# Performance work log

Hardware: AMD Instinct MI355X
Metric: run time of the kernel (lower is better)

The kernel has to match this reference:

```python
import jax, jax.numpy as jnp
import numpy as np

B, N, D = 4, 1024, 1024
H, HD = 16, 64  # num_heads, head_dim


def rotate_half(x):
    x1, x2 = jnp.split(x, 2, axis=-1)
    return jnp.concatenate([-x2, x1], axis=-1)


def setup_inputs() -> dict:
    key = jax.random.key(0)
    ks = jax.random.split(key, 10)
    s = 1.0 / np.sqrt(D)
    hidden_states = jax.random.normal(ks[0], (B, N, D), jnp.float32)
    # rotary angles -> cos/sin per position per head-dim
    ang = jax.random.uniform(ks[1], (B, N, HD), jnp.float32, 0.0, 2 * np.pi)
    cos, sin = jnp.cos(ang), jnp.sin(ang)
    wq = jax.random.normal(ks[2], (D, D), jnp.float32) * s
    bq = jnp.zeros((D,), jnp.float32)
    wk = jax.random.normal(ks[3], (D, D), jnp.float32) * s  # key_bias=False
    wv = jax.random.normal(ks[4], (D, D), jnp.float32) * s
    bv = jnp.zeros((D,), jnp.float32)
    wo = jax.random.normal(ks[5], (D, D), jnp.float32) * s
    bo = jnp.zeros((D,), jnp.float32)
    return {"hidden_states": hidden_states, "cos": cos, "sin": sin,
            "wq": wq, "bq": bq, "wk": wk, "wv": wv, "bv": bv,
            "wo": wo, "bo": bo}


def reference(hidden_states, cos, sin, wq, bq, wk, wv, bv, wo, bo):
    # weights are (out, in) as in eqx Linear: y = x @ W.T + b
    q = jnp.einsum('bnd,ed->bne', hidden_states, wq) + bq
    k = jnp.einsum('bnd,ed->bne', hidden_states, wk)
    v = jnp.einsum('bnd,ed->bne', hidden_states, wv) + bv
    # [B, H, N, HD]
    q = q.reshape(B, N, H, HD).transpose(0, 2, 1, 3)
    k = k.reshape(B, N, H, HD).transpose(0, 2, 1, 3)
    v = v.reshape(B, N, H, HD).transpose(0, 2, 1, 3)
    c = cos[:, None, :, :]  # broadcast over heads
    s = sin[:, None, :, :]
    q = q * c + rotate_half(q) * s
    k = k * c + rotate_half(k) * s
    scale = 1.0 / np.sqrt(HD)
    scores = jnp.einsum('bhqd,bhkd->bhqk', q, k) * scale
    attn = jax.nn.softmax(scores, axis=-1)
    out = jnp.einsum('bhqk,bhkd->bhqd', attn, v)
    out = out.transpose(0, 2, 1, 3).reshape(B, N, D)
    return jnp.einsum('bnd,ed->bne', out, wo) + bo
```

## Files before the change

### kernel.cpp

```cpp
#include <hip/hip_runtime.h>
#include <hip/hip_bf16.h>
#include <cstdint>


typedef _Float16 half8 __attribute__((ext_vector_type(8)));
typedef _Float16 half4 __attribute__((ext_vector_type(4)));
typedef float f32x4 __attribute__((ext_vector_type(4)));

#define DEV_INLINE __device__ __forceinline__

constexpr int Bb = 4, Ns = 1024, Dd = 1024, Hh = 16, HDd = 64;
constexpr int M_ROWS = Bb * Ns;
constexpr int EQKV = 3 * Dd;

constexpr size_t OFF_HSH  = 0;
constexpr size_t SZ_HSH   = (size_t)M_ROWS * Dd * 2;
constexpr size_t OFF_WQKV = OFF_HSH + SZ_HSH;
constexpr size_t SZ_WQKV  = (size_t)EQKV * Dd * 2;
constexpr size_t OFF_WO   = OFF_WQKV + SZ_WQKV;
constexpr size_t SZ_WO    = (size_t)Dd * Dd * 2;
constexpr size_t OFF_BIAS = OFF_WO + SZ_WO;
constexpr size_t OFF_VR   = OFF_BIAS + 16384;
constexpr size_t SZ_HEADS = (size_t)Bb * Hh * Ns * HDd * 2;
constexpr size_t OFF_QT   = OFF_VR + SZ_HEADS;
constexpr size_t OFF_KT   = OFF_QT + SZ_HEADS;
constexpr size_t OFF_VT   = OFF_KT + SZ_HEADS;
constexpr size_t OFF_ATTN = OFF_VR;

DEV_INLINE void async_cp16(const _Float16* g, _Float16* l) {
  __builtin_amdgcn_global_load_lds(
      (const __attribute__((address_space(1))) unsigned int*)(g),
      (__attribute__((address_space(3))) unsigned int*)(l), 16, 0, 0);
}

DEV_INLINE half4 cvt4(float4 v) {
  half4 h;
  h[0] = (_Float16)v.x; h[1] = (_Float16)v.y;
  h[2] = (_Float16)v.z; h[3] = (_Float16)v.w;
  return h;
}

__global__ __launch_bounds__(256) void cvt_kernel(
    const float* __restrict__ hs, const float* __restrict__ wq,
    const float* __restrict__ wk, const float* __restrict__ wv,
    const float* __restrict__ wo, const float* __restrict__ bq,
    const float* __restrict__ bv, _Float16* __restrict__ hsH,
    _Float16* __restrict__ wqkvH, _Float16* __restrict__ woH,
    float* __restrict__ biasP)
{
  const int gid = blockIdx.x * 256 + threadIdx.x;
  const int nHs4 = M_ROWS * Dd / 4;
  const int nW4  = 3 * Dd * Dd / 4;
  const int nWo4 = Dd * Dd / 4;
  if (gid < EQKV / 4) {
#pragma unroll
    for (int j = 0; j < 4; ++j) {
      int e = gid * 4 + j;
      biasP[e] = (e < 1024) ? bq[e] : (e < 2048 ? 0.f : bv[e - 2048]);
    }
  }
  if (gid < nHs4) {
    float4 v = reinterpret_cast<const float4*>(hs)[gid];
    reinterpret_cast<half4*>(hsH)[gid] = cvt4(v);
  } else if (gid < nHs4 + nW4) {
    int j = gid - nHs4;
    const int per = Dd * Dd / 4;
    const float* src = (j < per) ? wq : (j < 2 * per ? wk : wv);
    float4 v = reinterpret_cast<const float4*>(src)[j % per];
    reinterpret_cast<half4*>(wqkvH)[j] = cvt4(v);
  } else if (gid < nHs4 + nW4 + nWo4) {
    int j = gid - nHs4 - nW4;
    float4 v = reinterpret_cast<const float4*>(wo)[j];
    reinterpret_cast<half4*>(woH)[j] = cvt4(v);
  }
}

template<int MODE>
__global__ __launch_bounds__(256, 3) void gemm_bt(
    const _Float16* __restrict__ A, const _Float16* __restrict__ Bt,
    const float* __restrict__ bias, void* __restrict__ out,
    const float* __restrict__ cosp, const float* __restrict__ sinp,
    _Float16* __restrict__ qT, _Float16* __restrict__ kT,
    int M, int E, int K)
{
  __shared__ _Float16 As[128 * 64];
  __shared__ _Float16 Bs[128 * 64];
  const int t = threadIdx.x;
  const int lane = t & 63, wave = t >> 6;
  const int c15 = lane & 15, g = lane >> 4;
  const int wm = wave >> 1, wn = wave & 1;
  const int m0 = blockIdx.y * 128, e0 = blockIdx.x * 128;

  const int srow  = t >> 3;
  const int scol8 = ((t & 7) ^ ((t >> 3) & 7)) * 8;
  const _Float16* gA0 = A  + (size_t)(m0 + srow) * K + scol8;
  const _Float16* gB0 = Bt + (size_t)(e0 + srow) * K + scol8;
  char* lA = (char*)As + wave * 1024;
  char* lB = (char*)Bs + wave * 1024;

  const char* pA[4][2];
  const char* pB[4][2];
#pragma unroll
  for (int mi = 0; mi < 4; ++mi)
#pragma unroll
    for (int kh = 0; kh < 2; ++kh) {
      int ra = wm * 64 + mi * 16 + c15;
      pA[mi][kh] = (const char*)As + ra * 128 + (((kh * 4 + g) ^ (ra & 7)) << 4);
      int rb = wn * 64 + mi * 16 + c15;
      pB[mi][kh] = (const char*)Bs + rb * 128 + (((kh * 4 + g) ^ (rb & 7)) << 4);
    }

  f32x4 acc[4][4];
  const f32x4 zero = {0.f, 0.f, 0.f, 0.f};
#pragma unroll
  for (int i = 0; i < 4; ++i)
#pragma unroll
    for (int j = 0; j < 4; ++j) acc[i][j] = zero;

  const int nk = K >> 6;
  for (int kt = 0; kt < nk; ++kt) {
    const _Float16* ga = gA0 + kt * 64;
    const _Float16* gb = gB0 + kt * 64;
#pragma unroll
    for (int i = 0; i < 4; ++i) {
      async_cp16(ga + (size_t)(32 * i) * K, (_Float16*)(lA + i * 4096));
      async_cp16(gb + (size_t)(32 * i) * K, (_Float16*)(lB + i * 4096));
    }
    __syncthreads();
#pragma unroll
    for (int kh = 0; kh < 2; ++kh) {
      half8 a[4], b[4];
#pragma unroll
      for (int i = 0; i < 4; ++i) a[i] = *reinterpret_cast<const half8*>(pA[i][kh]);
#pragma unroll
      for (int i = 0; i < 4; ++i) b[i] = *reinterpret_cast<const half8*>(pB[i][kh]);
#pragma unroll
      for (int i = 0; i < 4; ++i)
#pragma unroll
        for (int j = 0; j < 4; ++j)
          acc[i][j] = __builtin_amdgcn_mfma_f32_16x16x32_f16(a[i], b[j], acc[i][j], 0, 0, 0);
    }
    __syncthreads();
  }

  if (MODE == 1) {
#pragma unroll
    for (int i = 0; i < 4; ++i)
#pragma unroll
      for (int j = 0; j < 4; ++j)
#pragma unroll
        for (int r = 0; r < 4; ++r) {
          int row = m0 + wm * 64 + i * 16 + g * 4 + r;
          int col = e0 + wn * 64 + j * 16 + c15;
          reinterpret_cast<float*>(out)[(size_t)row * E + col] =
              acc[i][j][r] + bias[col];
        }
  } else {
    const int scol = e0 + wn * 64;
    const int sec = scol >> 10;
    const int h = (scol & 1023) >> 6;
    if (sec < 2) {
      _Float16* dst = sec ? kT : qT;
#pragma unroll
      for (int i = 0; i < 4; ++i)
#pragma unroll
        for (int r = 0; r < 4; ++r) {
          int row = m0 + wm * 64 + i * 16 + g * 4 + r;
          int bh = (row >> 10) * Hh + h;
          size_t obase = ((size_t)bh * Ns + (row & 1023)) * HDd;
          const float* cb = cosp + (size_t)row * HDd;
          const float* sb = sinp + (size_t)row * HDd;
#pragma unroll
          for (int j = 0; j < 2; ++j) {
            int hd = j * 16 + c15;
            float x1 = acc[i][j][r]     + bias[scol + hd];
            float x2 = acc[i][j + 2][r] + bias[scol + hd + 32];
            float c1 = cb[hd],      s1 = sb[hd];
            float c2 = cb[hd + 32], s2 = sb[hd + 32];
            dst[obase + hd]      = (_Float16)(x1 * c1 - x2 * s1);
            dst[obase + hd + 32] = (_Float16)(x2 * c2 + x1 * s2);
          }
        }
    } else {
      _Float16* vR = (_Float16*)out;
#pragma unroll
      for (int i = 0; i < 4; ++i)
#pragma unroll
        for (int r = 0; r < 4; ++r) {
          int row = m0 + wm * 64 + i * 16 + g * 4 + r;
          int bh = (row >> 10) * Hh + h;
          size_t obase = ((size_t)bh * Ns + (row & 1023)) * HDd;
#pragma unroll
          for (int j = 0; j < 4; ++j) {
            int hd = j * 16 + c15;
            vR[obase + hd] = (_Float16)(acc[i][j][r] + bias[scol + hd]);
          }
        }
    }
  }
}

__global__ __launch_bounds__(256) void vtrans_kernel(
    const _Float16* __restrict__ vR, _Float16* __restrict__ vTo)
{
  __shared__ _Float16 Vs[64 * 72];
  const int t = threadIdx.x;
  const int bx = blockIdx.x;
  const int nt = bx & 15, bh = bx >> 4;
  const int n0 = nt * 64;
#pragma unroll
  for (int ii = 0; ii < 2; ++ii) {
    int cid = t + 256 * ii;
    int r = cid >> 3, ch = cid & 7;
    half8 v = *reinterpret_cast<const half8*>(
        vR + ((size_t)bh * Ns + n0 + r) * HDd + ch * 8);
    *reinterpret_cast<half8*>(&Vs[r * 72 + ch * 8]) = v;
  }
  __syncthreads();
#pragma unroll
  for (int ii = 0; ii < 2; ++ii) {
    int cid = t + 256 * ii;
    int d = cid >> 3, ch = cid & 7;
    half8 w;
#pragma unroll
    for (int kk = 0; kk < 8; ++kk) w[kk] = Vs[(ch * 8 + kk) * 72 + d];
    *reinterpret_cast<half8*>(vTo + ((size_t)bh * HDd + d) * Ns + n0 + ch * 8) = w;
  }
}

__global__ __launch_bounds__(256, 2) void attn_kernel(
    const _Float16* __restrict__ qT, const _Float16* __restrict__ kT,
    const _Float16* __restrict__ vT, _Float16* __restrict__ attnH)
{
  __shared__ _Float16 Ks[2][64 * 64];
  __shared__ _Float16 Vst[2][64 * 64];
  __shared__ _Float16 Ps[128 * 64];
  const int t = threadIdx.x;
  const int lane = t & 63, wave = t >> 6;
  const int c = lane & 15, g = lane >> 4;
  const int bx = blockIdx.x;
  const int qt = bx & 7, bh = bx >> 3;
  const int b = bh >> 4, h = bh & 15;
  const int qn0 = qt * 128;
  const int wq0 = wave * 32;

  half8 qf[2][2];
#pragma unroll
  for (int s16 = 0; s16 < 2; ++s16) {
    const _Float16* qp =
        qT + ((size_t)bh * Ns + qn0 + wq0 + s16 * 16 + c) * HDd + g * 8;
    qf[s16][0] = *reinterpret_cast<const half8*>(qp);
    qf[s16][1] = *reinterpret_cast<const half8*>(qp + 32);
  }

  half8 ones;
#pragma unroll
  for (int j = 0; j < 8; ++j) ones[j] = (_Float16)1.0f;

  f32x4 accO[2][4];
  f32x4 accL[2];
  const f32x4 zero = {0.f, 0.f, 0.f, 0.f};
#pragma unroll
  for (int s16 = 0; s16 < 2; ++s16) {
    accL[s16] = zero;
#pragma unroll
    for (int d = 0; d < 4; ++d) accO[s16][d] = zero;
  }

  const int srow = t >> 3, sch = t & 7;
  const int ssw = (sch * 16) ^ ((srow & 7) << 4);
  const _Float16* gK = kT + ((size_t)bh * Ns + srow) * HDd + sch * 8;
  const _Float16* gV = vT + ((size_t)bh * HDd + srow) * Ns + sch * 8;
  char* wKa = (char*)Ks[0]  + srow * 128 + ssw;
  char* wVa = (char*)Vst[0] + srow * 128 + ssw;

  const char* pK[2][4];
  const char* pV[2][4];
  const char* pP[2][2];
#pragma unroll
  for (int ks = 0; ks < 2; ++ks) {
#pragma unroll
    for (int i = 0; i < 4; ++i) {
      int rowk = i * 16 + c;
      pK[ks][i] = (const char*)Ks[0]  + rowk * 128 + ((ks * 64 + g * 16) ^ ((rowk & 7) << 4));
      pV[ks][i] = (const char*)Vst[0] + rowk * 128 + ((ks * 64 + g * 16) ^ ((rowk & 7) << 4));
    }
#pragma unroll
    for (int s16 = 0; s16 < 2; ++s16) {
      int rowp = wq0 + s16 * 16 + c;
      pP[s16][ks] = (const char*)Ps + rowp * 128 + ((ks * 64 + g * 16) ^ ((rowp & 7) << 4));
    }
  }

  const float K1 = 0.18033688011112042f;
  const float K2 = -11.541560327111707f;
  char* prow0 = (char*)Ps + (wq0 + c) * 128;
  const int psw = (c & 7) << 4;

  {
    half8 k0 = *reinterpret_cast<const half8*>(gK);
    half8 k1 = *reinterpret_cast<const half8*>(gK + 32 * HDd);
    half8 v0 = *reinterpret_cast<const half8*>(gV);
    half8 v1 = *reinterpret_cast<const half8*>(gV + 32 * Ns);
    *reinterpret_cast<half8*>(wKa) = k0;
    *reinterpret_cast<half8*>(wKa + 4096) = k1;
    *reinterpret_cast<half8*>(wVa) = v0;
    *reinterpret_cast<half8*>(wVa + 4096) = v1;
  }
  __syncthreads();

  for (int jt = 0; jt < 16; ++jt) {
    const int bo = (jt & 1) * 8192;
    const bool pre = (jt + 1 < 16);
    half8 kr0, kr1, vr0, vr1;
    if (pre) {
      kr0 = *reinterpret_cast<const half8*>(gK + (jt + 1) * 4096);
      kr1 = *reinterpret_cast<const half8*>(gK + (jt + 1) * 4096 + 32 * HDd);
      vr0 = *reinterpret_cast<const half8*>(gV + (jt + 1) * 64);
      vr1 = *reinterpret_cast<const half8*>(gV + (jt + 1) * 64 + 32 * Ns);
    }

    f32x4 s[2][4];
#pragma unroll
    for (int s16 = 0; s16 < 2; ++s16)
#pragma unroll
      for (int i = 0; i < 4; ++i) s[s16][i] = zero;
    __builtin_amdgcn_s_setprio(1);
#pragma unroll
    for (int ks = 0; ks < 2; ++ks) {
      half8 kf[4];
#pragma unroll
      for (int i = 0; i < 4; ++i)
        kf[i] = *reinterpret_cast<const half8*>(pK[ks][i] + bo);
#pragma unroll
      for (int i = 0; i < 4; ++i) {
        s[0][i] = __builtin_amdgcn_mfma_f32_16x16x32_f16(kf[i], qf[0][ks], s[0][i], 0, 0, 0);
        s[1][i] = __builtin_amdgcn_mfma_f32_16x16x32_f16(kf[i], qf[1][ks], s[1][i], 0, 0, 0);
      }
    }
    __builtin_amdgcn_s_setprio(0);

#pragma unroll
    for (int s16 = 0; s16 < 2; ++s16) {
      char* prow = prow0 + s16 * 2048;
#pragma unroll
      for (int i = 0; i < 4; ++i) {
        half4 pk;
        pk[0] = (_Float16)__builtin_amdgcn_exp2f(fmaf(s[s16][i][0], K1, K2));
        pk[1] = (_Float16)__builtin_amdgcn_exp2f(fmaf(s[s16][i][1], K1, K2));
        pk[2] = (_Float16)__builtin_amdgcn_exp2f(fmaf(s[s16][i][2], K1, K2));
        pk[3] = (_Float16)__builtin_amdgcn_exp2f(fmaf(s[s16][i][3], K1, K2));
        *reinterpret_cast<half4*>(prow + ((i * 32 + g * 8) ^ psw)) = pk;
      }
    }

    __builtin_amdgcn_s_setprio(1);
#pragma unroll
    for (int ks = 0; ks < 2; ++ks) {
      half8 pa0 = *reinterpret_cast<const half8*>(pP[0][ks]);
      half8 pa1 = *reinterpret_cast<const half8*>(pP[1][ks]);
      accL[0] = __builtin_amdgcn_mfma_f32_16x16x32_f16(pa0, ones, accL[0], 0, 0, 0);
      accL[1] = __builtin_amdgcn_mfma_f32_16x16x32_f16(pa1, ones, accL[1], 0, 0, 0);
#pragma unroll
      for (int dt = 0; dt < 4; ++dt) {
        half8 vf = *reinterpret_cast<const half8*>(pV[ks][dt] + bo);
        accO[0][dt] = __builtin_amdgcn_mfma_f32_16x16x32_f16(pa0, vf, accO[0][dt], 0, 0, 0);
        accO[1][dt] = __builtin_amdgcn_mfma_f32_16x16x32_f16(pa1, vf, accO[1][dt], 0, 0, 0);
      }
    }
    __builtin_amdgcn_s_setprio(0);

    if (pre) {
      const int wo_ = 8192 - bo;
      *reinterpret_cast<half8*>(wKa + wo_) = kr0;
      *reinterpret_cast<half8*>(wKa + wo_ + 4096) = kr1;
      *reinterpret_cast<half8*>(wVa + wo_) = vr0;
      *reinterpret_cast<half8*>(wVa + wo_ + 4096) = vr1;
      __syncthreads();
    }
  }

#pragma unroll
  for (int s16 = 0; s16 < 2; ++s16)
#pragma unroll
    for (int r = 0; r < 4; ++r) {
      float inv = 1.f / accL[s16][r];
      int n = qn0 + wq0 + s16 * 16 + g * 4 + r;
#pragma unroll
      for (int dt = 0; dt < 4; ++dt) {
        float v = accO[s16][dt][r] * inv;
        attnH[((size_t)b * Ns + n) * Dd + h * HDd + dt * 16 + c] = (_Float16)v;
      }
    }
}

extern "C" void kernel_launch(void* const* d_in, const int* in_sizes, int n_in,
                              void* d_out, int out_size, void* d_ws, size_t ws_size,
                              hipStream_t stream) {
  const float* hs   = (const float*)d_in[0];
  const float* cosp = (const float*)d_in[1];
  const float* sinp = (const float*)d_in[2];
  const float* wq   = (const float*)d_in[3];
  const float* bq   = (const float*)d_in[4];
  const float* wk   = (const float*)d_in[5];
  const float* wv   = (const float*)d_in[6];
  const float* bv   = (const float*)d_in[7];
  const float* wo   = (const float*)d_in[8];
  const float* bo   = (const float*)d_in[9];

  char* ws = (char*)d_ws;
  _Float16* hsH   = (_Float16*)(ws + OFF_HSH);
  _Float16* wqkvH = (_Float16*)(ws + OFF_WQKV);
  _Float16* woH   = (_Float16*)(ws + OFF_WO);
  float*    biasP = (float*)(ws + OFF_BIAS);
  _Float16* vRp   = (_Float16*)(ws + OFF_VR);
  _Float16* qTp   = (_Float16*)(ws + OFF_QT);
  _Float16* kTp   = (_Float16*)(ws + OFF_KT);
  _Float16* vTp   = (_Float16*)(ws + OFF_VT);
  _Float16* attnH = (_Float16*)(ws + OFF_ATTN);

  cvt_kernel<<<8192, 256, 0, stream>>>(hs, wq, wk, wv, wo, bq, bv,
                                       hsH, wqkvH, woH, biasP);
  gemm_bt<0><<<dim3(EQKV / 128, M_ROWS / 128), 256, 0, stream>>>(
      hsH, wqkvH, biasP, vRp, cosp, sinp, qTp, kTp, M_ROWS, EQKV, Dd);
  vtrans_kernel<<<Bb * Hh * (Ns / 64), 256, 0, stream>>>(vRp, vTp);
  attn_kernel<<<Bb * Hh * (Ns / 128), 256, 0, stream>>>(qTp, kTp, vTp, attnH);
  gemm_bt<1><<<dim3(Dd / 128, M_ROWS / 128), 256, 0, stream>>>(
      attnH, woH, bo, d_out, nullptr, nullptr, nullptr, nullptr,
      M_ROWS, Dd, Dd);
}
```

Before: 102.4 us.

## Fuse V transpose into QKV GEMM epilogue and narrow output GEMM tile

```diff
diff --git a/kernel.cpp b/kernel.cpp
--- a/kernel.cpp
+++ b/kernel.cpp
@@ -20,12 +20,11 @@
 constexpr size_t OFF_WO   = OFF_WQKV + SZ_WQKV;
 constexpr size_t SZ_WO    = (size_t)Dd * Dd * 2;
 constexpr size_t OFF_BIAS = OFF_WO + SZ_WO;
-constexpr size_t OFF_VR   = OFF_BIAS + 16384;
+constexpr size_t OFF_ATTN = OFF_BIAS + 16384;
 constexpr size_t SZ_HEADS = (size_t)Bb * Hh * Ns * HDd * 2;
-constexpr size_t OFF_QT   = OFF_VR + SZ_HEADS;
+constexpr size_t OFF_QT   = OFF_ATTN + SZ_HEADS;
 constexpr size_t OFF_KT   = OFF_QT + SZ_HEADS;
 constexpr size_t OFF_VT   = OFF_KT + SZ_HEADS;
-constexpr size_t OFF_ATTN = OFF_VR;
 
 DEV_INLINE void async_cp16(const _Float16* g, _Float16* l) {
   __builtin_amdgcn_global_load_lds(
@@ -75,7 +74,7 @@
   }
 }
 
-template<int MODE>
+template<int MODE, int BN>
 __global__ __launch_bounds__(256, 3) void gemm_bt(
     const _Float16* __restrict__ A, const _Float16* __restrict__ Bt,
     const float* __restrict__ bias, void* __restrict__ out,
@@ -83,13 +82,14 @@
     _Float16* __restrict__ qT, _Float16* __restrict__ kT,
     int M, int E, int K)
 {
+  constexpr int JW = BN / 32;
   __shared__ _Float16 As[128 * 64];
-  __shared__ _Float16 Bs[128 * 64];
+  __shared__ _Float16 Bs[BN * 64];
   const int t = threadIdx.x;
   const int lane = t & 63, wave = t >> 6;
   const int c15 = lane & 15, g = lane >> 4;
   const int wm = wave >> 1, wn = wave & 1;
-  const int m0 = blockIdx.y * 128, e0 = blockIdx.x * 128;
+  const int m0 = blockIdx.y * 128, e0 = blockIdx.x * BN;
 
   const int srow  = t >> 3;
   const int scol8 = ((t & 7) ^ ((t >> 3) & 7)) * 8;
@@ -99,45 +99,51 @@
   char* lB = (char*)Bs + wave * 1024;
 
   const char* pA[4][2];
-  const char* pB[4][2];
+  const char* pB[JW][2];
 #pragma unroll
   for (int mi = 0; mi < 4; ++mi)
 #pragma unroll
     for (int kh = 0; kh < 2; ++kh) {
       int ra = wm * 64 + mi * 16 + c15;
       pA[mi][kh] = (const char*)As + ra * 128 + (((kh * 4 + g) ^ (ra & 7)) << 4);
-      int rb = wn * 64 + mi * 16 + c15;
-      pB[mi][kh] = (const char*)Bs + rb * 128 + (((kh * 4 + g) ^ (rb & 7)) << 4);
-    }
-
-  f32x4 acc[4][4];
+    }
+#pragma unroll
+  for (int j = 0; j < JW; ++j)
+#pragma unroll
+    for (int kh = 0; kh < 2; ++kh) {
+      int rb = wn * (BN / 2) + j * 16 + c15;
+      pB[j][kh] = (const char*)Bs + rb * 128 + (((kh * 4 + g) ^ (rb & 7)) << 4);
+    }
+
+  f32x4 acc[4][JW];
   const f32x4 zero = {0.f, 0.f, 0.f, 0.f};
 #pragma unroll
   for (int i = 0; i < 4; ++i)
 #pragma unroll
-    for (int j = 0; j < 4; ++j) acc[i][j] = zero;
+    for (int j = 0; j < JW; ++j) acc[i][j] = zero;
 
   const int nk = K >> 6;
   for (int kt = 0; kt < nk; ++kt) {
     const _Float16* ga = gA0 + kt * 64;
     const _Float16* gb = gB0 + kt * 64;
 #pragma unroll
-    for (int i = 0; i < 4; ++i) {
+    for (int i = 0; i < 4; ++i)
       async_cp16(ga + (size_t)(32 * i) * K, (_Float16*)(lA + i * 4096));
+#pragma unroll
+    for (int i = 0; i < BN / 32; ++i)
       async_cp16(gb + (size_t)(32 * i) * K, (_Float16*)(lB + i * 4096));
-    }
     __syncthreads();
 #pragma unroll
     for (int kh = 0; kh < 2; ++kh) {
-      half8 a[4], b[4];
+      half8 a[4], b[JW];
 #pragma unroll
       for (int i = 0; i < 4; ++i) a[i] = *reinterpret_cast<const half8*>(pA[i][kh]);
 #pragma unroll
-      for (int i = 0; i < 4; ++i) b[i] = *reinterpret_cast<const half8*>(pB[i][kh]);
+      for (int j = 0; j < JW; ++j) b[j] = *reinterpret_cast<const half8*>(pB[j][kh]);
 #pragma unroll
       for (int i = 0; i < 4; ++i)
 #pragma unroll
-        for (int j = 0; j < 4; ++j)
+        for (int j = 0; j < JW; ++j)
           acc[i][j] = __builtin_amdgcn_mfma_f32_16x16x32_f16(a[i], b[j], acc[i][j], 0, 0, 0);
     }
     __syncthreads();
@@ -147,11 +153,11 @@
 #pragma unroll
     for (int i = 0; i < 4; ++i)
 #pragma unroll
-      for (int j = 0; j < 4; ++j)
+      for (int j = 0; j < JW; ++j)
 #pragma unroll
         for (int r = 0; r < 4; ++r) {
           int row = m0 + wm * 64 + i * 16 + g * 4 + r;
-          int col = e0 + wn * 64 + j * 16 + c15;
+          int col = e0 + wn * (BN / 2) + j * 16 + c15;
           reinterpret_cast<float*>(out)[(size_t)row * E + col] =
               acc[i][j][r] + bias[col];
         }
@@ -159,6 +165,7 @@
     const int scol = e0 + wn * 64;
     const int sec = scol >> 10;
     const int h = (scol & 1023) >> 6;
+    const int bh = (m0 >> 10) * Hh + h;
     if (sec < 2) {
       _Float16* dst = sec ? kT : qT;
 #pragma unroll
@@ -166,7 +173,6 @@
 #pragma unroll
         for (int r = 0; r < 4; ++r) {
           int row = m0 + wm * 64 + i * 16 + g * 4 + r;
-          int bh = (row >> 10) * Hh + h;
           size_t obase = ((size_t)bh * Ns + (row & 1023)) * HDd;
           const float* cb = cosp + (size_t)row * HDd;
           const float* sb = sinp + (size_t)row * HDd;
@@ -182,49 +188,20 @@
           }
         }
     } else {
-      _Float16* vR = (_Float16*)out;
+      _Float16* vTo = (_Float16*)out;
+      _Float16* vbase = vTo + (size_t)bh * (HDd * Ns) + (m0 & 1023) + wm * 64;
 #pragma unroll
       for (int i = 0; i < 4; ++i)
 #pragma unroll
-        for (int r = 0; r < 4; ++r) {
-          int row = m0 + wm * 64 + i * 16 + g * 4 + r;
-          int bh = (row >> 10) * Hh + h;
-          size_t obase = ((size_t)bh * Ns + (row & 1023)) * HDd;
-#pragma unroll
-          for (int j = 0; j < 4; ++j) {
-            int hd = j * 16 + c15;
-            vR[obase + hd] = (_Float16)(acc[i][j][r] + bias[scol + hd]);
-          }
+        for (int j = 0; j < 4; ++j) {
+          int hd = j * 16 + c15;
+          float bv_ = bias[scol + hd];
+          half4 pk;
+#pragma unroll
+          for (int r = 0; r < 4; ++r) pk[r] = (_Float16)(acc[i][j][r] + bv_);
+          *reinterpret_cast<half4*>(vbase + (size_t)hd * Ns + i * 16 + g * 4) = pk;
         }
     }
-  }
-}
-
-__global__ __launch_bounds__(256) void vtrans_kernel(
-    const _Float16* __restrict__ vR, _Float16* __restrict__ vTo)
-{
-  __shared__ _Float16 Vs[64 * 72];
-  const int t = threadIdx.x;
-  const int bx = blockIdx.x;
-  const int nt = bx & 15, bh = bx >> 4;
-  const int n0 = nt * 64;
-#pragma unroll
-  for (int ii = 0; ii < 2; ++ii) {
-    int cid = t + 256 * ii;
-    int r = cid >> 3, ch = cid & 7;
-    half8 v = *reinterpret_cast<const half8*>(
-        vR + ((size_t)bh * Ns + n0 + r) * HDd + ch * 8);
-    *reinterpret_cast<half8*>(&Vs[r * 72 + ch * 8]) = v;
-  }
-  __syncthreads();
-#pragma unroll
-  for (int ii = 0; ii < 2; ++ii) {
-    int cid = t + 256 * ii;
-    int d = cid >> 3, ch = cid & 7;
-    half8 w;
-#pragma unroll
-    for (int kk = 0; kk < 8; ++kk) w[kk] = Vs[(ch * 8 + kk) * 72 + d];
-    *reinterpret_cast<half8*>(vTo + ((size_t)bh * HDd + d) * Ns + n0 + ch * 8) = w;
   }
 }
 
@@ -413,19 +390,17 @@
   _Float16* wqkvH = (_Float16*)(ws + OFF_WQKV);
   _Float16* woH   = (_Float16*)(ws + OFF_WO);
   float*    biasP = (float*)(ws + OFF_BIAS);
-  _Float16* vRp   = (_Float16*)(ws + OFF_VR);
+  _Float16* attnH = (_Float16*)(ws + OFF_ATTN);
   _Float16* qTp   = (_Float16*)(ws + OFF_QT);
   _Float16* kTp   = (_Float16*)(ws + OFF_KT);
   _Float16* vTp   = (_Float16*)(ws + OFF_VT);
-  _Float16* attnH = (_Float16*)(ws + OFF_ATTN);
 
   cvt_kernel<<<8192, 256, 0, stream>>>(hs, wq, wk, wv, wo, bq, bv,
                                        hsH, wqkvH, woH, biasP);
-  gemm_bt<0><<<dim3(EQKV / 128, M_ROWS / 128), 256, 0, stream>>>(
-      hsH, wqkvH, biasP, vRp, cosp, sinp, qTp, kTp, M_ROWS, EQKV, Dd);
-  vtrans_kernel<<<Bb * Hh * (Ns / 64), 256, 0, stream>>>(vRp, vTp);
+  gemm_bt<0, 128><<<dim3(EQKV / 128, M_ROWS / 128), 256, 0, stream>>>(
+      hsH, wqkvH, biasP, vTp, cosp, sinp, qTp, kTp, M_ROWS, EQKV, Dd);
   attn_kernel<<<Bb * Hh * (Ns / 128), 256, 0, stream>>>(qTp, kTp, vTp, attnH);
-  gemm_bt<1><<<dim3(Dd / 128, M_ROWS / 128), 256, 0, stream>>>(
+  gemm_bt<1, 64><<<dim3(Dd / 64, M_ROWS / 128), 256, 0, stream>>>(
       attnH, woH, bo, d_out, nullptr, nullptr, nullptr, nullptr,
       M_ROWS, Dd, Dd);
 }
```

Measured after the change: 95.25 us. 7.0% less time.
